# Kernel optimization log

Measured on AMD Instinct MI355X. Metric: run time of the kernel, lower is better.

## Reference

```python
import jax, jax.numpy as jnp
import numpy as np

SCALE = 32.0  # hardcoded self.scale in the module


def fwht(x):
    """Fast Walsh-Hadamard transform along last dim (power-of-2 length).
    Equivalent to x @ H_n (Sylvester Hadamard), unnormalized."""
    orig_shape = x.shape
    n = orig_shape[-1]
    x = x.reshape(-1, n)
    h = 2
    while h <= n:
        x = x.reshape(-1, n // h, h)
        half = h // 2
        a = x[:, :, :half]
        b = x[:, :, half:]
        x = jnp.concatenate([a + b, a - b], axis=-1)
        h *= 2
    return x.reshape(orig_shape)


def setup_inputs() -> dict:
    key = jax.random.key(0)
    k1, k2, k3, k4, k5 = jax.random.split(key, 5)
    B, S, N, M = 8, 2048, 4096, 4096
    x = jax.random.normal(k1, (B, S, N), dtype=jnp.float32)
    W = jax.random.normal(k2, (M, N), dtype=jnp.float32) * 0.02  # nn.Linear weight [out, in]
    SU = jax.random.uniform(k3, (N,), dtype=jnp.float32, minval=0.5, maxval=1.5)
    SV = jax.random.uniform(k4, (M,), dtype=jnp.float32, minval=0.5, maxval=1.5)
    Wscale = jax.random.uniform(k5, (M,), dtype=jnp.float32, minval=0.5, maxval=1.5)
    return {"x": x, "W": W, "SU": SU, "SV": SV, "Wscale": Wscale}


def reference(x, W, SU, SV, Wscale):
    n = SU.shape[0]
    m = SV.shape[0]
    inv_sqrt_n = 1.0 / np.sqrt(n).astype(np.float32)
    inv_sqrt_m = 1.0 / np.sqrt(m).astype(np.float32)
    h = x.reshape(-1, n) * SU                       # per-channel input scale
    h = fwht(h) * (inv_sqrt_n / SCALE)              # normalized Hadamard rotation / scale
    h = jnp.einsum('tn,mn->tm', h, W) * Wscale      # linear + per-channel weight scale
    h = fwht(h) * inv_sqrt_m                        # inverse (normalized) Hadamard rotation
    h = h * (SV * SCALE)                            # per-channel output scale * scale
    return h.reshape(*x.shape[:-1], m)
```

## Files before the change

kernel.cpp:

```cpp
#include <hip/hip_runtime.h>
#include <hip/hip_bf16.h>

typedef __bf16 bf16x8 __attribute__((ext_vector_type(8)));
typedef float f32x4 __attribute__((ext_vector_type(4)));

__device__ __forceinline__ void gload16(const void* g, void* l) {
  __builtin_amdgcn_global_load_lds(
      (const __attribute__((address_space(1))) void*)g,
      (__attribute__((address_space(3))) void*)l, 16, 0, 0);
}

__device__ __forceinline__ unsigned short f2bf(float f) {
  __hip_bfloat16 h = __float2bfloat16(f);
  union { __hip_bfloat16 h; unsigned short u; } c;
  c.h = h;
  return c.u;
}

__device__ __forceinline__ void fwht16(float v[16]) {
#pragma unroll
  for (int s = 1; s < 16; s <<= 1) {
#pragma unroll
    for (int i = 0; i < 16; i++) {
      if ((i & s) == 0) {
        float a = v[i], b = v[i | s];
        v[i] = a + b;
        v[i | s] = a - b;
      }
    }
  }
}

__global__ __launch_bounds__(256) void fwht1_kernel(
    const float* __restrict__ x, const float* __restrict__ SU,
    unsigned short* __restrict__ H1) {
  __shared__ float lds[256 * 17];
  const int t = threadIdx.x;
  const size_t row = blockIdx.x;
  const float* xr = x + row * 4096;
  float v[16];
#pragma unroll
  for (int n2 = 0; n2 < 16; n2++) {
    int n = n2 * 256 + t;
    v[n2] = xr[n] * SU[n];
  }
  fwht16(v);
  const int n1 = t >> 4, n0 = t & 15;
#pragma unroll
  for (int j2 = 0; j2 < 16; j2++) lds[(j2 * 16 + n1) * 17 + n0] = v[j2];
  __syncthreads();
#pragma unroll
  for (int k = 0; k < 16; k++) v[k] = lds[((t >> 4) * 16 + k) * 17 + (t & 15)];
  fwht16(v);
#pragma unroll
  for (int k = 0; k < 16; k++) lds[((t >> 4) * 16 + k) * 17 + (t & 15)] = v[k];
  __syncthreads();
#pragma unroll
  for (int k = 0; k < 16; k++) v[k] = lds[t * 17 + k];
  fwht16(v);
  const float cst = 1.0f / 2048.0f;
  union { unsigned short u[16]; uint4 q[2]; } o;
#pragma unroll
  for (int k = 0; k < 16; k++) o.u[k] = f2bf(v[k] * cst);
  uint4* dst = (uint4*)(H1 + row * 4096 + (size_t)t * 16);
  dst[0] = o.q[0];
  dst[1] = o.q[1];
}

__global__ __launch_bounds__(256) void convw_kernel(
    const float4* __restrict__ W4, const float* __restrict__ Wscale,
    uint2* __restrict__ Wb4, int total4, int Nq) {
  int i = blockIdx.x * 256 + threadIdx.x;
  if (i >= total4) return;
  float4 w = W4[i];
  float s = Wscale[i / Nq];
  unsigned int lo = (unsigned)f2bf(w.x * s) | ((unsigned)f2bf(w.y * s) << 16);
  unsigned int hi = (unsigned)f2bf(w.z * s) | ((unsigned)f2bf(w.w * s) << 16);
  Wb4[i] = make_uint2(lo, hi);
}


#define BARRIER()                          \
  do {                                     \
    asm volatile("" ::: "memory");         \
    __builtin_amdgcn_s_barrier();          \
    asm volatile("" ::: "memory");         \
  } while (0)
#define GATE4() asm volatile("s_waitcnt vmcnt(4)" ::: "memory")
#define GATE8() asm volatile("s_waitcnt vmcnt(8)" ::: "memory")
#define GATE0() asm volatile("s_waitcnt vmcnt(0)" ::: "memory")

__device__ __forceinline__ void stage_half(const unsigned short* __restrict__ g,
                                           unsigned short* l, int tid, int K) {
#pragma unroll
  for (int i = 0; i < 2; i++) {
    int idx = i * 512 + tid;
    int r = idx >> 3;
    int c = (idx & 7) ^ (r & 7);
    gload16(g + (size_t)r * K + c * 8, l + idx * 8);
  }
}
__device__ __forceinline__ void stage_quarter(
    const unsigned short* __restrict__ g, unsigned short* l, int tid, int K) {
  int r = tid >> 3;
  int c = (tid & 7) ^ (r & 7);
  gload16(g + (size_t)r * K + c * 8, l + tid * 8);
}

#define STAGE_A(d, hh, kt) \
  stage_half(Abase + (size_t)(hh) * 128 * K + (size_t)(kt) * 64, &As[d][(hh) * 8192], tid, K)
#define STAGE_B(d, hh, kt) \
  stage_half(Bbase + (size_t)(hh) * 128 * K + (size_t)(kt) * 64, &Bs[d][(hh) * 8192], tid, K)
#define STAGE_AQ(d, q, kt) \
  stage_quarter(Abase + (size_t)(q) * 64 * K + (size_t)(kt) * 64, &As[d][(q) * 4096], tid, K)

#define LOAD_A(d, h)                                                          \
  {                                                                           \
    _Pragma("unroll") for (int i = 0; i < 4; i++) {                           \
      _Pragma("unroll") for (int ks = 0; ks < 2; ks++) {                      \
        int r = wm * 128 + (h) * 64 + i * 16 + fr;                            \
        int kc = ks * 4 + lhi;                                                \
        ah[i][ks] = *(const bf16x8*)&As[d][r * 64 + ((kc ^ (r & 7)) << 3)];   \
      }                                                                       \
    }                                                                         \
  }

#define LOAD_B(d, v, dst)                                                     \
  {                                                                           \
    _Pragma("unroll") for (int j = 0; j < 2; j++) {                           \
      _Pragma("unroll") for (int ks = 0; ks < 2; ks++) {                      \
        int r = wn * 64 + (v) * 32 + j * 16 + fr;                             \
        int kc = ks * 4 + lhi;                                                \
        dst[j][ks] = *(const bf16x8*)&Bs[d][r * 64 + ((kc ^ (r & 7)) << 3)];  \
      }                                                                       \
    }                                                                         \
  }

#define MFMA_PH(h, v, bvx)                                                    \
  {                                                                           \
    __builtin_amdgcn_s_setprio(1);                                            \
    _Pragma("unroll") for (int i = 0; i < 4; i++)                             \
      _Pragma("unroll") for (int j = 0; j < 2; j++)                           \
        _Pragma("unroll") for (int ks = 0; ks < 2; ks++)                      \
          acc[(h)*4 + i][(v)*2 + j] = __builtin_amdgcn_mfma_f32_16x16x32_bf16( \
              ah[i][ks], bvx[j][ks], acc[(h)*4 + i][(v)*2 + j], 0, 0, 0);     \
    __builtin_amdgcn_s_setprio(0);                                            \
  }

__global__ __launch_bounds__(512, 2) void gemm8_kernel(
    const unsigned short* __restrict__ A, const unsigned short* __restrict__ B,
    float* __restrict__ C, int M, int K, int NT) {
  __shared__ __align__(16) unsigned short As[2][256 * 64];
  __shared__ __align__(16) unsigned short Bs[2][256 * 64];
  const int nbn = M >> 8;
  const int cpx = gridDim.x >> 3;
  int bid = blockIdx.x;
  bid = (bid & 7) * cpx + (bid >> 3);
  const int brow = (bid / nbn) << 8;
  const int bcol = (bid % nbn) << 8;
  const int tid = threadIdx.x;
  const int lane = tid & 63;
  const int w = tid >> 6;
  const int wm = w >> 2;
  const int wn = w & 3;
  const int fr = lane & 15;
  const int lhi = lane >> 4;

  const unsigned short* Abase = A + (size_t)brow * K;
  const unsigned short* Bbase = B + (size_t)bcol * K;

  f32x4 acc[8][4];
#pragma unroll
  for (int i = 0; i < 8; i++)
#pragma unroll
    for (int j = 0; j < 4; j++) acc[i][j] = (f32x4){0.f, 0.f, 0.f, 0.f};
  bf16x8 ah[4][2], bvA[2][2], bvB[2][2], bv1[2][2];

  STAGE_A(0, 0, 0);
  STAGE_A(0, 1, 0);
  STAGE_B(0, 0, 0);
  STAGE_B(0, 1, 0);
  STAGE_A(1, 0, 1);
  STAGE_A(1, 1, 1);
  STAGE_B(1, 0, 1);
  STAGE_B(1, 1, 1);
  GATE8();
  BARRIER();
  LOAD_B(0, 0, bvA);

  const int NTT = NT / 2;
#pragma unroll 1
  for (int t = 0; t < NTT; ++t) {
    const bool last = (t == NTT - 1);
    const int u2 = 2 * t + 2, u3 = 2 * t + 3;
    LOAD_A(0, 0);
    BARRIER();
    MFMA_PH(0, 0, bvA);
    BARRIER();
    LOAD_B(0, 1, bv1);
    if (!last) { STAGE_AQ(0, 0, u2); STAGE_AQ(0, 2, u2); }
    BARRIER();
    MFMA_PH(0, 1, bv1);
    BARRIER();
    LOAD_A(0, 1);
    if (!last) STAGE_B(0, 0, u2);
    BARRIER();
    MFMA_PH(1, 1, bv1);
    BARRIER();
    if (!last) { GATE4(); } else { GATE0(); }
    LOAD_B(1, 0, bvB);
    if (!last) { STAGE_B(0, 1, u2); STAGE_AQ(0, 1, u2); STAGE_AQ(0, 3, u2); }
    BARRIER();
    MFMA_PH(1, 0, bvA);
    BARRIER();
    LOAD_A(1, 0);
    BARRIER();
    MFMA_PH(0, 0, bvB);
    BARRIER();
    LOAD_B(1, 1, bv1);
    if (!last) { STAGE_AQ(1, 0, u3); STAGE_AQ(1, 2, u3); }
    BARRIER();
    MFMA_PH(0, 1, bv1);
    BARRIER();
    LOAD_A(1, 1);
    if (!last) STAGE_B(1, 0, u3);
    BARRIER();
    MFMA_PH(1, 1, bv1);
    BARRIER();
    if (!last) {
      GATE4();
      LOAD_B(0, 0, bvA);
      STAGE_B(1, 1, u3);
      STAGE_AQ(1, 1, u3);
      STAGE_AQ(1, 3, u3);
    }
    BARRIER();
    MFMA_PH(1, 0, bvB);
    BARRIER();
  }

  const int crow0 = brow + wm * 128 + lhi * 4;
  const int ccol0 = bcol + wn * 64 + fr;
#pragma unroll
  for (int mi = 0; mi < 8; mi++)
#pragma unroll
    for (int nj = 0; nj < 4; nj++)
#pragma unroll
      for (int q = 0; q < 4; q++)
        C[(size_t)(crow0 + mi * 16 + q) * M + ccol0 + nj * 16] = acc[mi][nj][q];
}

__global__ __launch_bounds__(256) void fwht2_kernel(
    float* __restrict__ Y, const float* __restrict__ SV) {
  __shared__ float lds[256 * 17];
  const int t = threadIdx.x;
  const size_t row = blockIdx.x;
  float* yr = Y + row * 4096;
  float v[16];
#pragma unroll
  for (int n2 = 0; n2 < 16; n2++) v[n2] = yr[n2 * 256 + t];
  fwht16(v);
  const int n1 = t >> 4, n0 = t & 15;
#pragma unroll
  for (int j2 = 0; j2 < 16; j2++) lds[(j2 * 16 + n1) * 17 + n0] = v[j2];
  __syncthreads();
#pragma unroll
  for (int k = 0; k < 16; k++) v[k] = lds[((t >> 4) * 16 + k) * 17 + (t & 15)];
  fwht16(v);
#pragma unroll
  for (int k = 0; k < 16; k++) lds[((t >> 4) * 16 + k) * 17 + (t & 15)] = v[k];
  __syncthreads();
#pragma unroll
  for (int k = 0; k < 16; k++) v[k] = lds[t * 17 + k];
  fwht16(v);
  float outv[16];
#pragma unroll
  for (int k = 0; k < 16; k++) outv[k] = v[k] * 0.5f * SV[(size_t)t * 16 + k];
  float4* dst = (float4*)(yr + (size_t)t * 16);
#pragma unroll
  for (int k = 0; k < 4; k++)
    dst[k] = make_float4(outv[4 * k], outv[4 * k + 1], outv[4 * k + 2],
                         outv[4 * k + 3]);
}

extern "C" void kernel_launch(void* const* d_in, const int* in_sizes, int n_in,
                              void* d_out, int out_size, void* d_ws,
                              size_t ws_size, hipStream_t stream) {
  const float* x = (const float*)d_in[0];
  const float* W = (const float*)d_in[1];
  const float* SU = (const float*)d_in[2];
  const float* SV = (const float*)d_in[3];
  const float* Wscale = (const float*)d_in[4];
  const int N = in_sizes[2];
  const int M = in_sizes[3];
  const int T = in_sizes[0] / N;

  unsigned short* H1 = (unsigned short*)d_ws;
  unsigned short* Wb = H1 + (size_t)T * N;
  float* out = (float*)d_out;

  fwht1_kernel<<<T, 256, 0, stream>>>(x, SU, H1);
  const int total4 = (int)(((long)M * N) / 4);
  convw_kernel<<<(total4 + 255) / 256, 256, 0, stream>>>(
      (const float4*)W, Wscale, (uint2*)Wb, total4, N / 4);
  const int NT = N / 64;
  gemm8_kernel<<<(T / 256) * (M / 256), 512, 0, stream>>>(H1, Wb, out, M, N, NT);
  fwht2_kernel<<<T, 256, 0, stream>>>(out, SV);
}
```

Before: 761.8 us.

## Restructure GEMM LDS layout into quadrant halves and deepen load/MFMA pipeline

Changes the shared-memory staging so that each half of A and B holds the rows each warp group needs for one phase, interleaved across warps. Staging is then issued per half-tile instead of per quarter. The main loop is reordered to double-buffer A fragments in registers (ahA/ahB) and to place finer vmcnt gates after each MFMA phase. The aim is to overlap global-to-LDS staging and LDS reads more fully with MFMA work. The cost is more live registers and a more complex wait schedule that must stay correct on the final iteration.

```diff
diff --git a/kernel.cpp b/kernel.cpp
--- a/kernel.cpp
+++ b/kernel.cpp
@@ -86,41 +86,48 @@
     __builtin_amdgcn_s_barrier();          \
     asm volatile("" ::: "memory");         \
   } while (0)
+#define GATE10() asm volatile("s_waitcnt vmcnt(10)" ::: "memory")
+#define GATE8() asm volatile("s_waitcnt vmcnt(8)" ::: "memory")
 #define GATE4() asm volatile("s_waitcnt vmcnt(4)" ::: "memory")
-#define GATE8() asm volatile("s_waitcnt vmcnt(8)" ::: "memory")
+#define GATE2() asm volatile("s_waitcnt vmcnt(2)" ::: "memory")
 #define GATE0() asm volatile("s_waitcnt vmcnt(0)" ::: "memory")
 
-__device__ __forceinline__ void stage_half(const unsigned short* __restrict__ g,
-                                           unsigned short* l, int tid, int K) {
+__device__ __forceinline__ void stage_A(const unsigned short* __restrict__ Ab,
+                                        unsigned short* lr, int h, int kt,
+                                        int tid, int K) {
 #pragma unroll
   for (int i = 0; i < 2; i++) {
     int idx = i * 512 + tid;
-    int r = idx >> 3;
-    int c = (idx & 7) ^ (r & 7);
-    gload16(g + (size_t)r * K + c * 8, l + idx * 8);
-  }
-}
-__device__ __forceinline__ void stage_quarter(
-    const unsigned short* __restrict__ g, unsigned short* l, int tid, int K) {
-  int r = tid >> 3;
-  int c = (tid & 7) ^ (r & 7);
-  gload16(g + (size_t)r * K + c * 8, l + tid * 8);
-}
-
-#define STAGE_A(d, hh, kt) \
-  stage_half(Abase + (size_t)(hh) * 128 * K + (size_t)(kt) * 64, &As[d][(hh) * 8192], tid, K)
-#define STAGE_B(d, hh, kt) \
-  stage_half(Bbase + (size_t)(hh) * 128 * K + (size_t)(kt) * 64, &Bs[d][(hh) * 8192], tid, K)
-#define STAGE_AQ(d, q, kt) \
-  stage_quarter(Abase + (size_t)(q) * 64 * K + (size_t)(kt) * 64, &As[d][(q) * 4096], tid, K)
-
-#define LOAD_A(d, h)                                                          \
+    int rl = idx >> 3;
+    int c = (idx & 7) ^ (rl & 7);
+    int grow = (rl >> 6) * 128 + h * 64 + (rl & 63);
+    gload16(Ab + (size_t)grow * K + (size_t)kt * 64 + c * 8, lr + idx * 8);
+  }
+}
+__device__ __forceinline__ void stage_B(const unsigned short* __restrict__ Bb,
+                                        unsigned short* lr, int v, int kt,
+                                        int tid, int K) {
+#pragma unroll
+  for (int i = 0; i < 2; i++) {
+    int idx = i * 512 + tid;
+    int rl = idx >> 3;
+    int c = (idx & 7) ^ (rl & 7);
+    int gcol = (rl >> 5) * 64 + v * 32 + (rl & 31);
+    gload16(Bb + (size_t)gcol * K + (size_t)kt * 64 + c * 8, lr + idx * 8);
+  }
+}
+
+#define STAGE_A(d, h, kt) stage_A(Abase, &As[d][(h)*8192], (h), (kt), tid, K)
+#define STAGE_B(d, v, kt) stage_B(Bbase, &Bs[d][(v)*8192], (v), (kt), tid, K)
+
+#define LOAD_A(d, h, dst)                                                     \
   {                                                                           \
     _Pragma("unroll") for (int i = 0; i < 4; i++) {                           \
       _Pragma("unroll") for (int ks = 0; ks < 2; ks++) {                      \
-        int r = wm * 128 + (h) * 64 + i * 16 + fr;                            \
+        int rl = wm * 64 + i * 16 + fr;                                       \
         int kc = ks * 4 + lhi;                                                \
-        ah[i][ks] = *(const bf16x8*)&As[d][r * 64 + ((kc ^ (r & 7)) << 3)];   \
+        dst[i][ks] =                                                          \
+            *(const bf16x8*)&As[d][(h)*8192 + rl * 64 + ((kc ^ (rl & 7)) << 3)]; \
       }                                                                       \
     }                                                                         \
   }
@@ -129,21 +136,24 @@
   {                                                                           \
     _Pragma("unroll") for (int j = 0; j < 2; j++) {                           \
       _Pragma("unroll") for (int ks = 0; ks < 2; ks++) {                      \
-        int r = wn * 64 + (v) * 32 + j * 16 + fr;                             \
+        int rl = wn * 32 + j * 16 + fr;                                       \
         int kc = ks * 4 + lhi;                                                \
-        dst[j][ks] = *(const bf16x8*)&Bs[d][r * 64 + ((kc ^ (r & 7)) << 3)];  \
+        dst[j][ks] =                                                          \
+            *(const bf16x8*)&Bs[d][(v)*8192 + rl * 64 + ((kc ^ (rl & 7)) << 3)]; \
       }                                                                       \
     }                                                                         \
   }
 
-#define MFMA_PH(h, v, bvx)                                                    \
+#define MFMA_PH(ho, vo, aset, bset)                                           \
   {                                                                           \
     __builtin_amdgcn_s_setprio(1);                                            \
     _Pragma("unroll") for (int i = 0; i < 4; i++)                             \
       _Pragma("unroll") for (int j = 0; j < 2; j++)                           \
         _Pragma("unroll") for (int ks = 0; ks < 2; ks++)                      \
-          acc[(h)*4 + i][(v)*2 + j] = __builtin_amdgcn_mfma_f32_16x16x32_bf16( \
-              ah[i][ks], bvx[j][ks], acc[(h)*4 + i][(v)*2 + j], 0, 0, 0);     \
+          acc[(ho)*4 + i][(vo)*2 + j] =                                       \
+              __builtin_amdgcn_mfma_f32_16x16x32_bf16(                        \
+                  aset[i][ks], bset[j][ks], acc[(ho)*4 + i][(vo)*2 + j], 0,   \
+                  0, 0);                                                      \
     __builtin_amdgcn_s_setprio(0);                                            \
   }
 
@@ -174,68 +184,74 @@
   for (int i = 0; i < 8; i++)
 #pragma unroll
     for (int j = 0; j < 4; j++) acc[i][j] = (f32x4){0.f, 0.f, 0.f, 0.f};
-  bf16x8 ah[4][2], bvA[2][2], bvB[2][2], bv1[2][2];
+  bf16x8 ahA[4][2], ahB[4][2], bv0A[2][2], bv0B[2][2], bv1[2][2];
 
   STAGE_A(0, 0, 0);
-  STAGE_A(0, 1, 0);
   STAGE_B(0, 0, 0);
   STAGE_B(0, 1, 0);
+  STAGE_A(0, 1, 0);
   STAGE_A(1, 0, 1);
-  STAGE_A(1, 1, 1);
   STAGE_B(1, 0, 1);
   STAGE_B(1, 1, 1);
+  GATE10();
+  BARRIER();
+  LOAD_A(0, 0, ahA);
+  LOAD_B(0, 0, bv0A);
   GATE8();
   BARRIER();
-  LOAD_B(0, 0, bvA);
 
   const int NTT = NT / 2;
 #pragma unroll 1
   for (int t = 0; t < NTT; ++t) {
     const bool last = (t == NTT - 1);
-    const int u2 = 2 * t + 2, u3 = 2 * t + 3;
-    LOAD_A(0, 0);
-    BARRIER();
-    MFMA_PH(0, 0, bvA);
-    BARRIER();
+    const int u1 = 2 * t + 1, u2 = 2 * t + 2, u3 = 2 * t + 3;
     LOAD_B(0, 1, bv1);
-    if (!last) { STAGE_AQ(0, 0, u2); STAGE_AQ(0, 2, u2); }
-    BARRIER();
-    MFMA_PH(0, 1, bv1);
-    BARRIER();
-    LOAD_A(0, 1);
+    STAGE_A(1, 1, u1);
+    BARRIER();
+    MFMA_PH(0, 0, ahA, bv0A);
+    GATE8();
+    BARRIER();
+    LOAD_A(0, 1, ahB);
+    if (!last) STAGE_A(0, 0, u2);
+    BARRIER();
+    MFMA_PH(0, 1, ahA, bv1);
+    BARRIER();
     if (!last) STAGE_B(0, 0, u2);
     BARRIER();
-    MFMA_PH(1, 1, bv1);
-    BARRIER();
-    if (!last) { GATE4(); } else { GATE0(); }
-    LOAD_B(1, 0, bvB);
-    if (!last) { STAGE_B(0, 1, u2); STAGE_AQ(0, 1, u2); STAGE_AQ(0, 3, u2); }
-    BARRIER();
-    MFMA_PH(1, 0, bvA);
-    BARRIER();
-    LOAD_A(1, 0);
-    BARRIER();
-    MFMA_PH(0, 0, bvB);
+    MFMA_PH(1, 1, ahB, bv1);
+    if (!last) { GATE8(); } else { GATE4(); }
+    BARRIER();
+    LOAD_A(1, 0, ahA);
+    LOAD_B(1, 0, bv0B);
+    if (!last) STAGE_B(0, 1, u2);
+    BARRIER();
+    MFMA_PH(1, 0, ahB, bv0A);
+    if (!last) { GATE8(); } else { GATE2(); }
     BARRIER();
     LOAD_B(1, 1, bv1);
-    if (!last) { STAGE_AQ(1, 0, u3); STAGE_AQ(1, 2, u3); }
-    BARRIER();
-    MFMA_PH(0, 1, bv1);
-    BARRIER();
-    LOAD_A(1, 1);
+    if (!last) STAGE_A(0, 1, u2);
+    BARRIER();
+    MFMA_PH(0, 0, ahA, bv0B);
+    if (!last) { GATE8(); } else { GATE0(); }
+    BARRIER();
+    LOAD_A(1, 1, ahB);
+    if (!last) STAGE_A(1, 0, u3);
+    BARRIER();
+    MFMA_PH(0, 1, ahA, bv1);
+    BARRIER();
     if (!last) STAGE_B(1, 0, u3);
     BARRIER();
-    MFMA_PH(1, 1, bv1);
+    MFMA_PH(1, 1, ahB, bv1);
+    if (!last) GATE8();
     BARRIER();
     if (!last) {
-      GATE4();
-      LOAD_B(0, 0, bvA);
+      LOAD_A(0, 0, ahA);
+      LOAD_B(0, 0, bv0A);
       STAGE_B(1, 1, u3);
-      STAGE_AQ(1, 1, u3);
-      STAGE_AQ(1, 3, u3);
     }
     BARRIER();
-    MFMA_PH(1, 0, bvB);
+    MFMA_PH(1, 0, ahB, bv0B);
+    if (!last) GATE8();
     BARRIER();
   }
 
```

Measured after the change: 1.355 ms. +77.8%, slower.
